# Optimization experiments

Measured on AMD Instinct MI355X. Metric: run time of the kernel, lower is better.

## Reference

```python
import jax, jax.numpy as jnp
import numpy as np

B, N, H, L, K, R = 1024, 64, 128, 4, 16, 20
CUTOFF = 5.0
GAMMA = 10.0   # RBF width
N_TYPES = 10

def _rn(k, shape, scale):
    return jax.random.normal(k, shape, jnp.float32) * scale

def setup_inputs():
    key = jax.random.key(0)
    ks = jax.random.split(key, 16)
    z = lambda *s: jnp.zeros(s, jnp.float32)
    return {
        "positions": _rn(ks[0], (B, N, 3), 2.0),
        "atomic_numbers": jax.random.randint(ks[1], (B, N), 0, N_TYPES),
        "atom_embed": _rn(ks[2], (N_TYPES, H // 4), 0.1),
        "pos_W": _rn(ks[3], (3, 3 * H // 4), 0.5),
        "pos_b": z(3 * H // 4),
        "msg_W": _rn(ks[4], (L, 2 * H + R, H), (2 * H + R) ** -0.5),
        "msg_b": z(L, H),
        "upd_W": _rn(ks[5], (L, H, H), H ** -0.5),
        "upd_b": z(L, H),
        "gself_W": _rn(ks[6], (L, H, H), H ** -0.5),
        "gmean_W": _rn(ks[7], (L, H, H), H ** -0.5),
        "g_b": z(L, H),
        "fus_W": _rn(ks[8], (L, 2 * H, H), (2 * H) ** -0.5),
        "fus_b": z(L, H),
        "ln_g": jnp.ones((L, H), jnp.float32),
        "ln_b": z(L, H),
        "cb_W1": _rn(ks[9], (L, H, 4 * H), H ** -0.5),
        "cb_b1": z(L, 4 * H),
        "cb_W2": _rn(ks[10], (L, 4 * H, H), (4 * H) ** -0.5),
        "cb_b2": z(L, H),
        "fo_W1": _rn(ks[11], (H, H), H ** -0.5),
        "fo_b1": z(H),
        "fo_W2": _rn(ks[12], (H, 3), H ** -0.5),
        "fo_b2": z(3),
    }

def _ln(x, g, b):
    m = x.mean(-1, keepdims=True)
    v = ((x - m) ** 2).mean(-1, keepdims=True)
    return (x - m) * jax.lax.rsqrt(v + 1e-5) * g + b

def reference(positions, atomic_numbers, atom_embed, pos_W, pos_b, msg_W, msg_b,
              upd_W, upd_b, gself_W, gmean_W, g_b, fus_W, fus_b, ln_g, ln_b,
              cb_W1, cb_b1, cb_W2, cb_b2, fo_W1, fo_b1, fo_W2, fo_b2):
    silu = jax.nn.silu
    Bb, Nn, _ = positions.shape
    # embeddings: atom type (H/4) || position (3H/4)
    h = jnp.concatenate([atom_embed[atomic_numbers], positions @ pos_W + pos_b], -1)  # [B,N,H]
    # kNN graph from positions (static across layers since positions are fixed)
    diff = positions[:, :, None, :] - positions[:, None, :, :]
    d2 = jnp.sum(diff * diff, -1) + jnp.eye(Nn, dtype=positions.dtype) * 1e9  # exclude self
    neg_d2, idx = jax.lax.top_k(-d2, K)                       # [B,N,K]
    d = jnp.sqrt(jnp.maximum(-neg_d2, 1e-12))
    centers = jnp.linspace(0.0, CUTOFF, R).astype(positions.dtype)
    rbf = jnp.exp(-GAMMA * (d[..., None] - centers) ** 2)     # [B,N,K,R]
    env = (0.5 * (jnp.cos(jnp.pi * d / CUTOFF) + 1.0) * (d < CUTOFF))[..., None]  # cosine cutoff
    idx_flat = idx.reshape(Bb, Nn * K)
    for i in range(msg_W.shape[0]):
        # local MPNN: gather neighbors, message MLP on [h_i, h_j, rbf], envelope, sum
        h_j = jnp.take_along_axis(h, idx_flat[:, :, None], axis=1).reshape(Bb, Nn, K, -1)
        h_i = jnp.broadcast_to(h[:, :, None, :], h_j.shape)
        m = silu(jnp.concatenate([h_i, h_j, rbf], -1) @ msg_W[i] + msg_b[i]) * env
        local = h + silu(m.sum(2) @ upd_W[i] + upd_b[i])
        # Clifford mean-field: self transform + global-mean transform
        glob = silu(h @ gself_W[i] + h.mean(1, keepdims=True) @ gmean_W[i] + g_b[i])
        # fusion (dropout is identity at inference)
        fused = silu(jnp.concatenate([local, glob], -1) @ fus_W[i] + fus_b[i])
        # Clifford block: pre-LN residual MLP
        x = _ln(fused, ln_g[i], ln_b[i])
        h = fused + silu(x @ cb_W1[i] + cb_b1[i]) @ cb_W2[i] + cb_b2[i]
    return silu(h @ fo_W1 + fo_b1) @ fo_W2 + fo_b2  # [B,N,3] forces
```

## Files before the change

### kernel.cpp

```cpp
#include <hip/hip_runtime.h>

typedef unsigned short ushort_t;
typedef unsigned int uint_t;
typedef unsigned long long ull_t;
typedef __attribute__((ext_vector_type(8))) short short8;
typedef __attribute__((ext_vector_type(4))) float f32x4;

#define B_ 1024
#define N_ 64
#define H_ 128
#define NT 256

#define IMG_WI 0
#define IMG_WJ 16384
#define IMG_UW 32768
#define IMG_GS 49152
#define IMG_FT 65536
#define IMG_FB 81920
#define IMG_C1 98304
#define IMG_C2 163840
#define IMG_GMT 229376
#define IMG_RW 245760
#define IMG_L 249856
#define IMG_FO 999424
#define WS_WEIGHTS (2u*1024u*1024u)
#define KNN_STRIDE 12288u

__device__ __forceinline__ ushort_t f2bf(float f) {
    uint_t u = __float_as_uint(f);
    return (ushort_t)((u + 0x7fffu + ((u >> 16) & 1u)) >> 16);
}
__device__ __forceinline__ float bf2f(ushort_t u) {
    union { uint_t i; float f; } v; v.i = ((uint_t)u) << 16; return v.f;
}
__device__ __forceinline__ float siluf(float x) { return x / (1.0f + __expf(-x)); }

__device__ __forceinline__ int sidx(int m, int k) {
    return m * H_ + (((k >> 3) ^ (m & 7)) << 3) + (k & 7);
}
__device__ __forceinline__ int fragoff(int m, int ch) {
    return m * H_ + ((ch ^ (m & 7)) << 3);
}

extern "C" __global__ __launch_bounds__(256)
void convert_weights(const float* __restrict__ msg_W, const float* __restrict__ upd_W,
                     const float* __restrict__ gself_W, const float* __restrict__ fus_W,
                     const float* __restrict__ cb_W1, const float* __restrict__ cb_W2,
                     const float* __restrict__ gmean_W, const float* __restrict__ fo_W1,
                     ushort_t* __restrict__ wimg)
{
    const int g = blockIdx.x;
    if (g >= 244) {
        int st = g - 244;
        ushort_t* dst = wimg + IMG_FO + st * 4096;
        for (int e = 0; e < 16; ++e) {
            int q = threadIdx.x * 16 + e;
            int n = q >> 7, k = q & 127;
            dst[q] = f2bf(fo_W1[(size_t)k * 128 + st * 32 + n]);
        }
        return;
    }
    const int l = g / 61, r = g - l * 61;
    ushort_t* base = wimg + l * IMG_L;
    if (r == 60) {
        const float* W = msg_W + l * 35328 + 256 * 128;
        ushort_t* dst = base + IMG_RW;
        for (int e = 0; e < 16; ++e) {
            int q = threadIdx.x * 16 + e;
            int sub = q >> 10, n = (q >> 5) & 31, k = q & 31;
            dst[q] = f2bf(k < 20 ? W[(size_t)k * 128 + sub * 32 + n] : 0.0f);
        }
        return;
    }
    const float* W; int ld = 128, k0 = 0, c0, off, st;
    if      (r < 4)  { W = msg_W + l * 35328;            st = r;      off = IMG_WI;  c0 = st * 32; }
    else if (r < 8)  { W = msg_W + l * 35328;  k0 = 128; st = r - 4;  off = IMG_WJ;  c0 = st * 32; }
    else if (r < 12) { W = upd_W + l * 16384;            st = r - 8;  off = IMG_UW;  c0 = st * 32; }
    else if (r < 16) { W = gself_W + l * 16384;          st = r - 12; off = IMG_GS;  c0 = st * 32; }
    else if (r < 20) { W = fus_W + l * 32768;            st = r - 16; off = IMG_FT;  c0 = st * 32; }
    else if (r < 24) { W = fus_W + l * 32768;  k0 = 128; st = r - 20; off = IMG_FB;  c0 = st * 32; }
    else if (r < 40) { W = cb_W1 + l * 65536;  ld = 512; st = r - 24; off = IMG_C1;  c0 = st * 32; }
    else if (r < 56) { int j = (r - 40) >> 2; W = cb_W2 + l * 65536; k0 = j * 128;
                       st = r - 40; off = IMG_C2; c0 = ((r - 40) & 3) * 32; }
    else             { W = gmean_W + l * 16384;          st = r - 56; off = IMG_GMT; c0 = st * 32; }
    ushort_t* dst = base + off + st * 4096;
    for (int e = 0; e < 16; ++e) {
        int q = threadIdx.x * 16 + e;
        int n = q >> 7, k = q & 127;
        dst[q] = f2bf(W[(size_t)(k0 + k) * ld + c0 + n]);
    }
}

extern "C" __global__ __launch_bounds__(64)
void knn_kernel(const float* __restrict__ positions, char* __restrict__ ws)
{
    const int b = blockIdx.x, lane = threadIdx.x;
    float px = positions[b * 192 + lane * 3 + 0];
    float py = positions[b * 192 + lane * 3 + 1];
    float pz = positions[b * 192 + lane * 3 + 2];
    float* kd = (float*)(ws + WS_WEIGHTS + (size_t)b * KNN_STRIDE);
    float* ke = kd + 1024;
    ushort_t* ki = (ushort_t*)(ke + 1024);
    for (int n = 0; n < 64; ++n) {
        float dx = __fsub_rn(__shfl(px, n), px);
        float dy = __fsub_rn(__shfl(py, n), py);
        float dz = __fsub_rn(__shfl(pz, n), pz);
        float d2 = __fadd_rn(__fadd_rn(__fmul_rn(dx, dx), __fmul_rn(dy, dy)), __fmul_rn(dz, dz));
        if (lane == n) d2 = 1e30f;
        float sd = 0.f; int si = 0;
        for (int k = 0; k < 16; ++k) {
            float dmin = d2;
            #pragma unroll
            for (int o = 1; o < 64; o <<= 1) dmin = fminf(dmin, __shfl_xor(dmin, o));
            ull_t mask = __ballot(d2 == dmin);
            int widx = __ffsll(mask) - 1;
            if (lane == widx) d2 = 1e30f;
            if (lane == k) { si = widx; sd = dmin; }
        }
        if (lane < 16) {
            float dd = sqrtf(fmaxf(sd, 1e-12f));
            kd[n * 16 + lane] = dd;
            ke[n * 16 + lane] = (dd < 5.0f) ? 0.5f * (__cosf(0.62831853071795864769f * dd) + 1.0f) : 0.0f;
            ki[n * 16 + lane] = (ushort_t)si;
        }
    }
}

#define HFS 132
struct __align__(16) Smem {
    ushort_t T1[N_ * H_];
    ushort_t T2[N_ * H_];
    float Hf[N_ * HFS];
    float d[1024];
    float env[1024];
    ushort_t idx[1024];
    char u[2048];
};

__device__ __forceinline__ f32x4 gemm_s(const short8 a[4], const ushort_t* __restrict__ img,
                                        int s, int l15, int quad)
{
    const ushort_t* base = img + ((s >> 1) << 12) + ((((s & 1) << 4) + l15) << 7) + quad * 8;
    short8 b0 = *(const short8*)(base);
    short8 b1 = *(const short8*)(base + 32);
    short8 b2 = *(const short8*)(base + 64);
    short8 b3 = *(const short8*)(base + 96);
    f32x4 c = {0.f, 0.f, 0.f, 0.f};
    c = __builtin_amdgcn_mfma_f32_16x16x32_bf16(a[0], b0, c, 0, 0, 0);
    c = __builtin_amdgcn_mfma_f32_16x16x32_bf16(a[1], b1, c, 0, 0, 0);
    c = __builtin_amdgcn_mfma_f32_16x16x32_bf16(a[2], b2, c, 0, 0, 0);
    c = __builtin_amdgcn_mfma_f32_16x16x32_bf16(a[3], b3, c, 0, 0, 0);
    return c;
}
__device__ __forceinline__ f32x4 gemm_s_acc(const short8 a[4], const ushort_t* __restrict__ img,
                                            int s, int l15, int quad, f32x4 c)
{
    const ushort_t* base = img + ((s >> 1) << 12) + ((((s & 1) << 4) + l15) << 7) + quad * 8;
    short8 b0 = *(const short8*)(base);
    short8 b1 = *(const short8*)(base + 32);
    short8 b2 = *(const short8*)(base + 64);
    short8 b3 = *(const short8*)(base + 96);
    c = __builtin_amdgcn_mfma_f32_16x16x32_bf16(a[0], b0, c, 0, 0, 0);
    c = __builtin_amdgcn_mfma_f32_16x16x32_bf16(a[1], b1, c, 0, 0, 0);
    c = __builtin_amdgcn_mfma_f32_16x16x32_bf16(a[2], b2, c, 0, 0, 0);
    c = __builtin_amdgcn_mfma_f32_16x16x32_bf16(a[3], b3, c, 0, 0, 0);
    return c;
}
__device__ __forceinline__ void loadA(const ushort_t* __restrict__ X, int mrow, int quad, short8 a[4]) {
    #pragma unroll
    for (int kc = 0; kc < 4; ++kc) a[kc] = *(const short8*)&X[fragoff(mrow, kc * 4 + quad)];
}
__device__ __forceinline__ void buildA(const float* __restrict__ Hf, int mrow, int quad, short8 a[4]) {
    #pragma unroll
    for (int kc = 0; kc < 4; ++kc) {
        const float* p = Hf + mrow * HFS + (kc * 4 + quad) * 8;
        float4 u0 = *(const float4*)p;
        float4 u1 = *(const float4*)(p + 4);
        short8 v;
        v[0] = (short)f2bf(u0.x); v[1] = (short)f2bf(u0.y);
        v[2] = (short)f2bf(u0.z); v[3] = (short)f2bf(u0.w);
        v[4] = (short)f2bf(u1.x); v[5] = (short)f2bf(u1.y);
        v[6] = (short)f2bf(u1.z); v[7] = (short)f2bf(u1.w);
        a[kc] = v;
    }
}

extern "C" __global__ __launch_bounds__(NT, 2)
void md17_fused_kernel(
    const float* __restrict__ positions, const int* __restrict__ atomic_numbers,
    const float* __restrict__ atom_embed, const float* __restrict__ pos_W,
    const float* __restrict__ pos_b,
    const float* __restrict__ msg_b, const float* __restrict__ upd_b,
    const float* __restrict__ g_b, const float* __restrict__ fus_b,
    const float* __restrict__ ln_g, const float* __restrict__ ln_b,
    const float* __restrict__ cb_b1, const float* __restrict__ cb_b2,
    const float* __restrict__ fo_b1,
    const float* __restrict__ fo_W2, const float* __restrict__ fo_b2,
    char* __restrict__ ws, float* __restrict__ out)
{
    __shared__ Smem sm;
    const int b = blockIdx.x;
    const int tid = threadIdx.x;
    const int wave = tid >> 6, lane = tid & 63;
    const int quad = lane >> 4, l15 = lane & 15;
    const int mrow = wave * 16 + l15;
    const int rbase = wave * 16 + quad * 4;

    const ushort_t* wimg = (const ushort_t*)ws;
    float* spos = (float*)sm.u;
    ushort_t* part = (ushort_t*)sm.u;
    float* hmean = (float*)(sm.u + 1024);
    float* gvec  = (float*)(sm.u + 1536);

    {
        const char* kb = ws + WS_WEIGHTS + (size_t)b * KNN_STRIDE;
        const float* kd = (const float*)kb;
        const float* ke = (const float*)(kb + 4096);
        const uint_t* ki = (const uint_t*)(kb + 8192);
        for (int t = tid; t < 1024; t += NT) { sm.d[t] = kd[t]; sm.env[t] = ke[t]; }
        for (int t = tid; t < 512; t += NT) ((uint_t*)sm.idx)[t] = ki[t];
        if (tid < 192) spos[tid] = positions[b * 192 + tid];
    }
    __syncthreads();
    for (int t = tid; t < N_ * H_; t += NT) {
        int n = t >> 7, f = t & 127;
        float v;
        if (f < 32) {
            v = atom_embed[atomic_numbers[b * N_ + n] * 32 + f];
        } else {
            int j = f - 32;
            v = pos_b[j];
            #pragma unroll
            for (int c = 0; c < 3; ++c)
                v = fmaf(spos[n * 3 + c], pos_W[c * 96 + j], v);
        }
        sm.Hf[n * HFS + f] = v;
        sm.T1[sidx(n, f)] = f2bf(v);
    }
    __syncthreads();

    #pragma unroll 1
    for (int l = 0; l < 4; ++l) {
        const ushort_t* wl = wimg + l * IMG_L;
        const float* mb  = msg_b + l * H_;
        const float* ub  = upd_b + l * H_;
        const float* gb  = g_b + l * H_;
        const float* fb  = fus_b + l * H_;
        const float* lg  = ln_g + l * H_;
        const float* lb  = ln_b + l * H_;
        const float* c1b = cb_b1 + l * 4 * H_;
        const float* c2b = cb_b2 + l * H_;

        #pragma unroll
        for (int s = 0; s < 8; ++s) {
            int col = s * 16 + l15;
            const float* hp = sm.Hf + rbase * HFS + col;
            float p = hp[0] + hp[HFS] + hp[2 * HFS] + hp[3 * HFS];
            p += __shfl_xor(p, 16);
            p += __shfl_xor(p, 32);
            if (quad == 0) part[wave * 128 + col] = f2bf(p);
        }
        __syncthreads();
        if (tid < H_)
            hmean[tid] = (bf2f(part[tid]) + bf2f(part[128 + tid])
                        + bf2f(part[256 + tid]) + bf2f(part[384 + tid])) * (1.0f / 64.0f);
        __syncthreads();

        if (tid < H_) {
            float s = gb[tid];
            const ushort_t* wrow = wl + IMG_GMT + tid * 128;
            for (int c = 0; c < 128; c += 8) {
                short8 w = *(const short8*)(wrow + c);
                #pragma unroll
                for (int i = 0; i < 8; ++i) s = fmaf(hmean[c + i], bf2f((ushort_t)w[i]), s);
            }
            gvec[tid] = s;
        }
        {
            short8 a_h[4]; loadA(sm.T1, mrow, quad, a_h);
            #pragma unroll
            for (int s = 0; s < 8; ++s) {
                f32x4 c = gemm_s(a_h, wl + IMG_WI, s, l15, quad);
                int col = s * 16 + l15; float bv = mb[col];
                #pragma unroll
                for (int r = 0; r < 4; ++r)
                    sm.T1[sidx(rbase + r, col)] = f2bf(c[r] + bv);
            }
            #pragma unroll
            for (int s = 0; s < 8; ++s) {
                f32x4 c = gemm_s(a_h, wl + IMG_WJ, s, l15, quad);
                int col = s * 16 + l15;
                #pragma unroll
                for (int r = 0; r < 4; ++r)
                    sm.T2[sidx(rbase + r, col)] = f2bf(c[r]);
            }
        }
        __syncthreads();

        {
            float ccv[8];
            #pragma unroll
            for (int j = 0; j < 8; ++j)
                ccv[j] = (float)((double)(quad * 8 + j) * (5.0 / 19.0));
            #pragma unroll 1
            for (int g = 0; g < 16; ++g) {
                int n = wave * 16 + g;
                int jv[4]; float ev[4];
                #pragma unroll
                for (int r = 0; r < 4; ++r) {
                    int k = quad * 4 + r;
                    jv[r] = sm.idx[n * 16 + k];
                    ev[r] = sm.env[n * 16 + k];
                }
                float ddm = sm.d[n * 16 + l15];
                short8 arb;
                #pragma unroll
                for (int j = 0; j < 8; ++j) {
                    float t2 = ddm - ccv[j];
                    float rv = __expf(-10.0f * t2 * t2);
                    arb[j] = (short)((quad * 8 + j) < 20 ? f2bf(rv) : (ushort_t)0);
                }
                #pragma unroll
                for (int s = 0; s < 8; ++s) {
                    int col = s * 16 + l15;
                    const ushort_t* rbase_p = wl + IMG_RW + ((s >> 1) << 10)
                                            + ((((s & 1) << 4) + l15) << 5) + quad * 8;
                    short8 brw = *(const short8*)rbase_p;
                    f32x4 c = {0.f, 0.f, 0.f, 0.f};
                    c = __builtin_amdgcn_mfma_f32_16x16x32_bf16(arb, brw, c, 0, 0, 0);
                    float ai = bf2f(sm.T1[sidx(n, col)]);
                    float acc = 0.f;
                    #pragma unroll
                    for (int r = 0; r < 4; ++r) {
                        float gm = bf2f(sm.T2[sidx(jv[r], col)]);
                        acc = fmaf(siluf(ai + gm + c[r]), ev[r], acc);
                    }
                    acc += __shfl_xor(acc, 16);
                    acc += __shfl_xor(acc, 32);
                    if (quad == 0) sm.T1[sidx(n, col)] = f2bf(acc);
                }
            }
        }
        __syncthreads();


        {
            short8 a_m[4]; loadA(sm.T1, mrow, quad, a_m);
            #pragma unroll
            for (int s = 0; s < 8; ++s) {
                f32x4 c = gemm_s(a_m, wl + IMG_UW, s, l15, quad);
                int col = s * 16 + l15; float bv = ub[col];
                #pragma unroll
                for (int r = 0; r < 4; ++r)
                    sm.T2[sidx(rbase + r, col)] = f2bf(sm.Hf[(rbase + r) * HFS + col] + siluf(c[r] + bv));
            }
            short8 a_hh[4]; buildA(sm.Hf, mrow, quad, a_hh);
            #pragma unroll
            for (int s = 0; s < 8; ++s) {
                f32x4 c = gemm_s(a_hh, wl + IMG_GS, s, l15, quad);
                int col = s * 16 + l15; float gv = gvec[col];
                #pragma unroll
                for (int r = 0; r < 4; ++r)
                    sm.T1[sidx(rbase + r, col)] = f2bf(siluf(c[r] + gv));
            }
        }

        float sr[4] = {0.f, 0.f, 0.f, 0.f}, qr[4] = {0.f, 0.f, 0.f, 0.f};
        {
            short8 a_t[4];
            loadA(sm.T2, mrow, quad, a_t);
            #pragma unroll
            for (int s = 0; s < 8; ++s) {
                f32x4 c = gemm_s(a_t, wl + IMG_FT, s, l15, quad);
                int col = s * 16 + l15;
                int rb = rbase * HFS + col;
                sm.Hf[rb] = c[0]; sm.Hf[rb + HFS] = c[1];
                sm.Hf[rb + 2 * HFS] = c[2]; sm.Hf[rb + 3 * HFS] = c[3];
            }
            loadA(sm.T1, mrow, quad, a_t);
            #pragma unroll
            for (int s = 0; s < 8; ++s) {
                f32x4 c = gemm_s(a_t, wl + IMG_FB, s, l15, quad);
                int col = s * 16 + l15; float bv = fb[col];
                int rb = rbase * HFS + col;
                #pragma unroll
                for (int r = 0; r < 4; ++r) {
                    float v = siluf(sm.Hf[rb + r * HFS] + c[r] + bv);
                    sm.Hf[rb + r * HFS] = v;
                    sr[r] += v; qr[r] += v * v;
                }
            }
            #pragma unroll
            for (int o = 1; o < 16; o <<= 1) {
                #pragma unroll
                for (int r = 0; r < 4; ++r) {
                    sr[r] += __shfl_xor(sr[r], o);
                    qr[r] += __shfl_xor(qr[r], o);
                }
            }
        }

        #pragma unroll
        for (int r = 0; r < 4; ++r) {
            float mu = sr[r] * (1.0f / 128.0f);
            float var = qr[r] * (1.0f / 128.0f) - mu * mu;
            float rs = rsqrtf(var + 1e-5f);
            int row = rbase + r;
            #pragma unroll
            for (int s = 0; s < 8; ++s) {
                int col = s * 16 + l15;
                sm.T1[sidx(row, col)] = f2bf((sm.Hf[row * HFS + col] - mu) * rs * lg[col] + lb[col]);
            }
        }

        {
            short8 a_x[4]; loadA(sm.T1, mrow, quad, a_x);
            f32x4 acc2[8];
            #pragma unroll
            for (int s = 0; s < 8; ++s) acc2[s] = (f32x4){0.f, 0.f, 0.f, 0.f};
            #pragma unroll 1
            for (int j = 0; j < 4; ++j) {
                #pragma unroll
                for (int s = 0; s < 8; ++s) {
                    f32x4 c = gemm_s(a_x, wl + IMG_C1 + j * 16384, s, l15, quad);
                    int col = s * 16 + l15; float bv = c1b[j * H_ + col];
                    #pragma unroll
                    for (int r = 0; r < 4; ++r)
                        sm.T2[sidx(rbase + r, col)] = f2bf(siluf(c[r] + bv));
                }
                short8 a_t[4]; loadA(sm.T2, mrow, quad, a_t);
                #pragma unroll
                for (int s = 0; s < 8; ++s)
                    acc2[s] = gemm_s_acc(a_t, wl + IMG_C2 + j * 16384, s, l15, quad, acc2[s]);
            }
            #pragma unroll
            for (int s = 0; s < 8; ++s) {
                int col = s * 16 + l15; float bv = c2b[col];
                #pragma unroll
                for (int r = 0; r < 4; ++r) {
                    int row = rbase + r;
                    float v = sm.Hf[row * HFS + col] + acc2[s][r] + bv;
                    sm.Hf[row * HFS + col] = v;
                    sm.T1[sidx(row, col)] = f2bf(v);
                }
            }
        }
    }

    {
        short8 a_f[4]; loadA(sm.T1, mrow, quad, a_f);
        #pragma unroll
        for (int s = 0; s < 8; ++s) {
            f32x4 c = gemm_s(a_f, wimg + IMG_FO, s, l15, quad);
            int col = s * 16 + l15; float bv = fo_b1[col];
            #pragma unroll
            for (int r = 0; r < 4; ++r)
                sm.T2[sidx(rbase + r, col)] = f2bf(siluf(c[r] + bv));
        }
    }
    __syncthreads();
    if (tid < 192) {
        int n = tid / 3, j = tid - n * 3;
        float s = fo_b2[j];
        for (int c = 0; c < H_; ++c)
            s = fmaf(bf2f(sm.T2[sidx(n, c)]), fo_W2[c * 3 + j], s);
        out[b * 192 + tid] = s;
    }
}

extern "C" void kernel_launch(void* const* d_in, const int* in_sizes, int n_in,
                              void* d_out, int out_size, void* d_ws, size_t ws_size,
                              hipStream_t stream) {
    (void)in_sizes; (void)n_in; (void)out_size; (void)ws_size;
    convert_weights<<<248, 256, 0, stream>>>(
        (const float*)d_in[5], (const float*)d_in[7], (const float*)d_in[9],
        (const float*)d_in[12], (const float*)d_in[16], (const float*)d_in[18],
        (const float*)d_in[10], (const float*)d_in[20], (ushort_t*)d_ws);
    knn_kernel<<<B_, 64, 0, stream>>>((const float*)d_in[0], (char*)d_ws);
    md17_fused_kernel<<<B_, NT, 0, stream>>>(
        (const float*)d_in[0], (const int*)d_in[1],
        (const float*)d_in[2], (const float*)d_in[3], (const float*)d_in[4],
        (const float*)d_in[6], (const float*)d_in[8],
        (const float*)d_in[11], (const float*)d_in[13],
        (const float*)d_in[14], (const float*)d_in[15],
        (const float*)d_in[17], (const float*)d_in[19],
        (const float*)d_in[21],
        (const float*)d_in[22], (const float*)d_in[23],
        (char*)d_ws, (float*)d_out);
}
```

Measured before the change: 1.479 ms.

## Keep fp32 hidden state in registers and drop shared Hf buffer

Removes the 33KB fp32 hidden-state array from shared memory and keeps each thread's fp32 h tile (8x4) in registers across all layers. The gself GEMM now reuses the bf16 A fragment loaded once per layer, and the two fusion GEMMs are accumulated into a single MFMA chain instead of a round trip through shared memory. Launch bounds are raised to 3 blocks per CU to use the freed LDS, which adds register pressure and risks spills.

After: 1.727 ms. 1.17x slower.

```diff
diff --git a/kernel.cpp b/kernel.cpp
--- a/kernel.cpp
+++ b/kernel.cpp
@@ -126,11 +126,9 @@
     }
 }
 
-#define HFS 132
 struct __align__(16) Smem {
     ushort_t T1[N_ * H_];
     ushort_t T2[N_ * H_];
-    float Hf[N_ * HFS];
     float d[1024];
     float env[1024];
     ushort_t idx[1024];
@@ -170,22 +168,8 @@
     #pragma unroll
     for (int kc = 0; kc < 4; ++kc) a[kc] = *(const short8*)&X[fragoff(mrow, kc * 4 + quad)];
 }
-__device__ __forceinline__ void buildA(const float* __restrict__ Hf, int mrow, int quad, short8 a[4]) {
-    #pragma unroll
-    for (int kc = 0; kc < 4; ++kc) {
-        const float* p = Hf + mrow * HFS + (kc * 4 + quad) * 8;
-        float4 u0 = *(const float4*)p;
-        float4 u1 = *(const float4*)(p + 4);
-        short8 v;
-        v[0] = (short)f2bf(u0.x); v[1] = (short)f2bf(u0.y);
-        v[2] = (short)f2bf(u0.z); v[3] = (short)f2bf(u0.w);
-        v[4] = (short)f2bf(u1.x); v[5] = (short)f2bf(u1.y);
-        v[6] = (short)f2bf(u1.z); v[7] = (short)f2bf(u1.w);
-        a[kc] = v;
-    }
-}
-
-extern "C" __global__ __launch_bounds__(NT, 2)
+
+extern "C" __global__ __launch_bounds__(NT, 3)
 void md17_fused_kernel(
     const float* __restrict__ positions, const int* __restrict__ atomic_numbers,
     const float* __restrict__ atom_embed, const float* __restrict__ pos_W,
@@ -222,22 +206,32 @@
         if (tid < 192) spos[tid] = positions[b * 192 + tid];
     }
     __syncthreads();
-    for (int t = tid; t < N_ * H_; t += NT) {
-        int n = t >> 7, f = t & 127;
-        float v;
-        if (f < 32) {
-            v = atom_embed[atomic_numbers[b * N_ + n] * 32 + f];
-        } else {
-            int j = f - 32;
-            v = pos_b[j];
-            #pragma unroll
-            for (int c = 0; c < 3; ++c)
-                v = fmaf(spos[n * 3 + c], pos_W[c * 96 + j], v);
-        }
-        sm.Hf[n * HFS + f] = v;
-        sm.T1[sidx(n, f)] = f2bf(v);
-    }
-    __syncthreads();
+
+    float hreg[8][4];
+    {
+        int types[4];
+        #pragma unroll
+        for (int r = 0; r < 4; ++r) types[r] = atomic_numbers[b * N_ + rbase + r];
+        #pragma unroll
+        for (int s = 0; s < 8; ++s) {
+            int col = s * 16 + l15;
+            #pragma unroll
+            for (int r = 0; r < 4; ++r) {
+                int row = rbase + r;
+                float v;
+                if (col < 32) v = atom_embed[types[r] * 32 + col];
+                else {
+                    int j = col - 32;
+                    v = pos_b[j];
+                    #pragma unroll
+                    for (int c = 0; c < 3; ++c)
+                        v = fmaf(spos[row * 3 + c], pos_W[c * 96 + j], v);
+                }
+                hreg[s][r] = v;
+                sm.T1[sidx(row, col)] = f2bf(v);
+            }
+        }
+    }
 
     #pragma unroll 1
     for (int l = 0; l < 4; ++l) {
@@ -253,12 +247,10 @@
 
         #pragma unroll
         for (int s = 0; s < 8; ++s) {
-            int col = s * 16 + l15;
-            const float* hp = sm.Hf + rbase * HFS + col;
-            float p = hp[0] + hp[HFS] + hp[2 * HFS] + hp[3 * HFS];
+            float p = hreg[s][0] + hreg[s][1] + hreg[s][2] + hreg[s][3];
             p += __shfl_xor(p, 16);
             p += __shfl_xor(p, 32);
-            if (quad == 0) part[wave * 128 + col] = f2bf(p);
+            if (quad == 0) part[wave * 128 + s * 16 + l15] = f2bf(p);
         }
         __syncthreads();
         if (tid < H_)
@@ -266,6 +258,7 @@
                         + bf2f(part[256 + tid]) + bf2f(part[384 + tid])) * (1.0f / 64.0f);
         __syncthreads();
 
+        short8 a_h[4]; loadA(sm.T1, mrow, quad, a_h);
         if (tid < H_) {
             float s = gb[tid];
             const ushort_t* wrow = wl + IMG_GMT + tid * 128;
@@ -276,24 +269,21 @@
             }
             gvec[tid] = s;
         }
-        {
-            short8 a_h[4]; loadA(sm.T1, mrow, quad, a_h);
-            #pragma unroll
-            for (int s = 0; s < 8; ++s) {
-                f32x4 c = gemm_s(a_h, wl + IMG_WI, s, l15, quad);
-                int col = s * 16 + l15; float bv = mb[col];
-                #pragma unroll
-                for (int r = 0; r < 4; ++r)
-                    sm.T1[sidx(rbase + r, col)] = f2bf(c[r] + bv);
-            }
-            #pragma unroll
-            for (int s = 0; s < 8; ++s) {
-                f32x4 c = gemm_s(a_h, wl + IMG_WJ, s, l15, quad);
-                int col = s * 16 + l15;
-                #pragma unroll
-                for (int r = 0; r < 4; ++r)
-                    sm.T2[sidx(rbase + r, col)] = f2bf(c[r]);
-            }
+        #pragma unroll
+        for (int s = 0; s < 8; ++s) {
+            f32x4 c = gemm_s(a_h, wl + IMG_WI, s, l15, quad);
+            int col = s * 16 + l15; float bv = mb[col];
+            #pragma unroll
+            for (int r = 0; r < 4; ++r)
+                sm.T1[sidx(rbase + r, col)] = f2bf(c[r] + bv);
+        }
+        #pragma unroll
+        for (int s = 0; s < 8; ++s) {
+            f32x4 c = gemm_s(a_h, wl + IMG_WJ, s, l15, quad);
+            int col = s * 16 + l15;
+            #pragma unroll
+            for (int r = 0; r < 4; ++r)
+                sm.T2[sidx(rbase + r, col)] = f2bf(c[r]);
         }
         __syncthreads();
 
@@ -323,9 +313,9 @@
                 #pragma unroll
                 for (int s = 0; s < 8; ++s) {
                     int col = s * 16 + l15;
-                    const ushort_t* rbase_p = wl + IMG_RW + ((s >> 1) << 10)
-                                            + ((((s & 1) << 4) + l15) << 5) + quad * 8;
-                    short8 brw = *(const short8*)rbase_p;
+                    const ushort_t* rp = wl + IMG_RW + ((s >> 1) << 10)
+                                       + ((((s & 1) << 4) + l15) << 5) + quad * 8;
+                    short8 brw = *(const short8*)rp;
                     f32x4 c = {0.f, 0.f, 0.f, 0.f};
                     c = __builtin_amdgcn_mfma_f32_16x16x32_bf16(arb, brw, c, 0, 0, 0);
                     float ai = bf2f(sm.T1[sidx(n, col)]);
@@ -344,6 +334,7 @@
         __syncthreads();
 
 
+        short8 a_loc[4], a_gl[4];
         {
             short8 a_m[4]; loadA(sm.T1, mrow, quad, a_m);
             #pragma unroll
@@ -352,51 +343,39 @@
                 int col = s * 16 + l15; float bv = ub[col];
                 #pragma unroll
                 for (int r = 0; r < 4; ++r)
-                    sm.T2[sidx(rbase + r, col)] = f2bf(sm.Hf[(rbase + r) * HFS + col] + siluf(c[r] + bv));
-            }
-            short8 a_hh[4]; buildA(sm.Hf, mrow, quad, a_hh);
+                    sm.T2[sidx(rbase + r, col)] = f2bf(hreg[s][r] + siluf(c[r] + bv));
+            }
+            loadA(sm.T2, mrow, quad, a_loc);
             #pragma unroll
             for (int s = 0; s < 8; ++s) {
-                f32x4 c = gemm_s(a_hh, wl + IMG_GS, s, l15, quad);
+                f32x4 c = gemm_s(a_h, wl + IMG_GS, s, l15, quad);
                 int col = s * 16 + l15; float gv = gvec[col];
                 #pragma unroll
                 for (int r = 0; r < 4; ++r)
                     sm.T1[sidx(rbase + r, col)] = f2bf(siluf(c[r] + gv));
             }
+            loadA(sm.T1, mrow, quad, a_gl);
         }
 
         float sr[4] = {0.f, 0.f, 0.f, 0.f}, qr[4] = {0.f, 0.f, 0.f, 0.f};
-        {
-            short8 a_t[4];
-            loadA(sm.T2, mrow, quad, a_t);
-            #pragma unroll
-            for (int s = 0; s < 8; ++s) {
-                f32x4 c = gemm_s(a_t, wl + IMG_FT, s, l15, quad);
-                int col = s * 16 + l15;
-                int rb = rbase * HFS + col;
-                sm.Hf[rb] = c[0]; sm.Hf[rb + HFS] = c[1];
-                sm.Hf[rb + 2 * HFS] = c[2]; sm.Hf[rb + 3 * HFS] = c[3];
-            }
-            loadA(sm.T1, mrow, quad, a_t);
-            #pragma unroll
-            for (int s = 0; s < 8; ++s) {
-                f32x4 c = gemm_s(a_t, wl + IMG_FB, s, l15, quad);
-                int col = s * 16 + l15; float bv = fb[col];
-                int rb = rbase * HFS + col;
-                #pragma unroll
-                for (int r = 0; r < 4; ++r) {
-                    float v = siluf(sm.Hf[rb + r * HFS] + c[r] + bv);
-                    sm.Hf[rb + r * HFS] = v;
-                    sr[r] += v; qr[r] += v * v;
-                }
-            }
-            #pragma unroll
-            for (int o = 1; o < 16; o <<= 1) {
-                #pragma unroll
-                for (int r = 0; r < 4; ++r) {
-                    sr[r] += __shfl_xor(sr[r], o);
-                    qr[r] += __shfl_xor(qr[r], o);
-                }
+        #pragma unroll
+        for (int s = 0; s < 8; ++s) {
+            f32x4 c = gemm_s(a_loc, wl + IMG_FT, s, l15, quad);
+            c = gemm_s_acc(a_gl, wl + IMG_FB, s, l15, quad, c);
+            int col = s * 16 + l15; float bv = fb[col];
+            #pragma unroll
+            for (int r = 0; r < 4; ++r) {
+                float v = siluf(c[r] + bv);
+                hreg[s][r] = v;
+                sr[r] += v; qr[r] += v * v;
+            }
+        }
+        #pragma unroll
+        for (int o = 1; o < 16; o <<= 1) {
+            #pragma unroll
+            for (int r = 0; r < 4; ++r) {
+                sr[r] += __shfl_xor(sr[r], o);
+                qr[r] += __shfl_xor(qr[r], o);
             }
         }
 
@@ -409,7 +388,7 @@
             #pragma unroll
             for (int s = 0; s < 8; ++s) {
                 int col = s * 16 + l15;
-                sm.T1[sidx(row, col)] = f2bf((sm.Hf[row * HFS + col] - mu) * rs * lg[col] + lb[col]);
+                sm.T1[sidx(row, col)] = f2bf((hreg[s][r] - mu) * rs * lg[col] + lb[col]);
             }
         }
 
@@ -438,10 +417,9 @@
                 int col = s * 16 + l15; float bv = c2b[col];
                 #pragma unroll
                 for (int r = 0; r < 4; ++r) {
-                    int row = rbase + r;
-                    float v = sm.Hf[row * HFS + col] + acc2[s][r] + bv;
-                    sm.Hf[row * HFS + col] = v;
-                    sm.T1[sidx(row, col)] = f2bf(v);
+                    float v = hreg[s][r] + acc2[s][r] + bv;
+                    hreg[s][r] = v;
+                    sm.T1[sidx(rbase + r, col)] = f2bf(v);
                 }
             }
         }
```
